# Kernel tuning notes

Hardware: AMD Instinct MI355X
Metric: run time of the kernel (lower is better)

## Reference

```python
import jax, jax.numpy as jnp
import numpy as np

N, R, H, L, E = 50000, 16, 32, 8, 1600000


def setup_inputs() -> dict:
    key = jax.random.key(0)
    ks = jax.random.split(key, 8)
    edge_index = jax.random.randint(ks[0], (2, E), 0, N, dtype=jnp.int32)
    edge_type = jax.random.randint(ks[1], (E,), 0, R, dtype=jnp.int32)
    W1 = jax.random.normal(ks[2], (R, N, H), jnp.float32) * 0.02
    root1 = jax.random.normal(ks[3], (N, H), jnp.float32) * 0.02
    b1 = jnp.zeros((H,), jnp.float32)
    W2 = jax.random.normal(ks[4], (R, H, L), jnp.float32) * 0.1
    root2 = jax.random.normal(ks[5], (H, L), jnp.float32) * 0.1
    b2 = jnp.zeros((L,), jnp.float32)
    return {"edge_index": edge_index, "edge_type": edge_type,
            "W1": W1, "root1": root1, "b1": b1,
            "W2": W2, "root2": root2, "b2": b2}


def reference(edge_index, edge_type, W1, root1, b1, W2, root2, b2):
    src, dst = edge_index[0], edge_index[1]
    # PyG RGCNConv uses mean aggregation per relation: segment = (relation, dst)
    seg = edge_type * N + dst                                   # [E]
    cnt = jax.ops.segment_sum(jnp.ones((E,), jnp.float32), seg, num_segments=R * N)
    norm_e = (1.0 / jnp.maximum(cnt, 1.0))[seg]                 # per-edge 1/deg_r(dst)

    # Layer 1: x is None -> message for edge (j->i, r) is W1[r, j]; root term is root1[i]
    msg1 = W1[edge_type, src] * norm_e[:, None]                 # [E, H]
    agg1 = jax.ops.segment_sum(msg1, dst, num_segments=N)       # [N, H]
    h1 = jax.nn.relu(agg1 + root1 + b1)

    # Layer 2: mean-aggregate h1[src] per (relation, dst), then relation-wise GEMM
    msg2 = h1[src] * norm_e[:, None]                            # [E, H]
    A = jax.ops.segment_sum(msg2, seg, num_segments=R * N).reshape(R, N, H)
    out = jnp.einsum('rnh,rhl->nl', A, W2) + h1 @ root2 + b2    # [N, L]
    return jax.nn.sigmoid(out)
```

## Files before the change

### kernel.cpp

```cpp
#include <hip/hip_runtime.h>
#include <hip/hip_bf16.h>

#define Nn 50000
#define Rr 16
#define Hh 32
#define Ll 8
#define Ee 1600000
#define NSEG 800000
#define NB 782
#define CH 4096
#define NBLK1 391
#define COLS 392
#define HT_INT4 76636
#define CAP 3072
#define W2U 20

typedef _Float16 h2 __attribute__((ext_vector_type(2)));

__device__ __forceinline__ float dot2(h2 a, unsigned b, float c) {
#ifdef __AMDGCN__
    return __builtin_amdgcn_fdot2(a, __builtin_bit_cast(h2, b), c, false);
#else
    h2 hb = __builtin_bit_cast(h2, b);
    return fmaf((float)a[0], (float)hb[0],
                fmaf((float)a[1], (float)hb[1], c));
#endif
}

__global__ __launch_bounds__(256) void p1hist_kernel(
        const int* __restrict__ dst, int* __restrict__ histT) {
    __shared__ int hist[1024];
    for (int i = threadIdx.x; i < 1024; i += 256) hist[i] = 0;
    __syncthreads();
    int base = blockIdx.x * CH;
    int n = min(CH, Ee - base);
    for (int i = threadIdx.x; i < n; i += 256)
        atomicAdd(&hist[dst[base + i] >> 6], 1);
    __syncthreads();
    for (int k = threadIdx.x; k < NB; k += 256)
        histT[k * COLS + blockIdx.x] = hist[k];
}

__global__ __launch_bounds__(256) void scan1_kernel(
        int4* data4, int* __restrict__ bsum) {
    __shared__ int sm[256];
    int i4 = blockIdx.x * 256 + threadIdx.x;
    int4 v = make_int4(0, 0, 0, 0);
    if (i4 < HT_INT4) v = data4[i4];
    int s0 = v.x, s1 = s0 + v.y, s2 = s1 + v.z, s3 = s2 + v.w;
    sm[threadIdx.x] = s3;
    __syncthreads();
    for (int off = 1; off < 256; off <<= 1) {
        int add = (threadIdx.x >= off) ? sm[threadIdx.x - off] : 0;
        __syncthreads();
        sm[threadIdx.x] += add;
        __syncthreads();
    }
    int base = sm[threadIdx.x] - s3;
    if (i4 < HT_INT4)
        data4[i4] = make_int4(base, base + s0, base + s1, base + s2);
    if (threadIdx.x == 255) bsum[blockIdx.x] = sm[255];
}

__global__ __launch_bounds__(1024) void scan2_kernel(
        const int* __restrict__ bsum, int* __restrict__ boff, int nblk) {
    __shared__ int sm[1024];
    int v = (threadIdx.x < nblk) ? bsum[threadIdx.x] : 0;
    sm[threadIdx.x] = v;
    __syncthreads();
    for (int off = 1; off < 1024; off <<= 1) {
        int add = (threadIdx.x >= off) ? sm[threadIdx.x - off] : 0;
        __syncthreads();
        sm[threadIdx.x] += add;
        __syncthreads();
    }
    if (threadIdx.x < nblk) boff[threadIdx.x] = sm[threadIdx.x] - v;
}

__global__ __launch_bounds__(256) void p1scat_kernel(
        const int* __restrict__ src, const int* __restrict__ dst,
        const int* __restrict__ etype, const int* __restrict__ offsT,
        const int* __restrict__ boff, unsigned* __restrict__ pay) {
    __shared__ int lhist[1024], lofs[1024], lcur[1024], goff[1024];
    __shared__ int partial[256];
    __shared__ unsigned stage[CH];
    __shared__ unsigned short sbkt[CH];
    int t = threadIdx.x;
    for (int i = t; i < 1024; i += 256) lhist[i] = 0;
    __syncthreads();
    int base = blockIdx.x * CH;
    int n = min(CH, Ee - base);
    for (int i = t; i < n; i += 256)
        atomicAdd(&lhist[dst[base + i] >> 6], 1);
    __syncthreads();
    int h0 = lhist[4*t], h1v = lhist[4*t+1], h2i = lhist[4*t+2], h3 = lhist[4*t+3];
    int s = h0 + h1v + h2i + h3;
    partial[t] = s;
    __syncthreads();
    for (int off = 1; off < 256; off <<= 1) {
        int add = (t >= off) ? partial[t - off] : 0;
        __syncthreads();
        partial[t] += add;
        __syncthreads();
    }
    int run = partial[t] - s;
    lofs[4*t] = run; lcur[4*t] = run; run += h0;
    lofs[4*t+1] = run; lcur[4*t+1] = run; run += h1v;
    lofs[4*t+2] = run; lcur[4*t+2] = run; run += h2i;
    lofs[4*t+3] = run; lcur[4*t+3] = run;
    for (int k = t; k < NB; k += 256) {
        int idx = k * COLS + blockIdx.x;
        goff[k] = offsT[idx] + boff[idx >> 10];
    }
    __syncthreads();
    for (int i = t; i < n; i += 256) {
        int e = base + i;
        int dv = dst[e];
        int b = dv >> 6;
        int pos = atomicAdd(&lcur[b], 1);
        stage[pos] = ((unsigned)(dv & 63) << 20) | ((unsigned)etype[e] << 16)
                   | (unsigned)src[e];
        sbkt[pos] = (unsigned short)b;
    }
    __syncthreads();
    for (int j = t; j < n; j += 256) {
        int b = sbkt[j];
        pay[goff[b] + (j - lofs[b])] = stage[j];
    }
}

__global__ __launch_bounds__(256) void p2sort_kernel(
        const int* __restrict__ offsT, const int* __restrict__ boff,
        unsigned* pay, unsigned* __restrict__ combo) {
    __shared__ unsigned buf[CAP], outb[CAP];
    __shared__ int hist[1024], lofs[1024], lcur[1024], partial[256];
    int k = blockIdx.x, t = threadIdx.x;
    int idx0 = k * COLS;
    int base = offsT[idx0] + boff[idx0 >> 10];
    int next;
    if (k == NB - 1) {
        next = Ee;
    } else {
        int idx1 = (k + 1) * COLS;
        next = offsT[idx1] + boff[idx1 >> 10];
    }
    int n = next - base;
    for (int i = t; i < 1024; i += 256) hist[i] = 0;
    __syncthreads();
    for (int j = t; j < n; j += 256) {
        unsigned p = pay[base + j];
        buf[j] = p;
        atomicAdd(&hist[(p >> 16) & 0x3FFu], 1);
    }
    __syncthreads();
    int h0 = hist[4*t], h1v = hist[4*t+1], h2i = hist[4*t+2], h3 = hist[4*t+3];
    int s = h0 + h1v + h2i + h3;
    partial[t] = s;
    __syncthreads();
    for (int off = 1; off < 256; off <<= 1) {
        int add = (t >= off) ? partial[t - off] : 0;
        __syncthreads();
        partial[t] += add;
        __syncthreads();
    }
    int run = partial[t] - s;
    lofs[4*t] = run; lcur[4*t] = run; run += h0;
    lofs[4*t+1] = run; lcur[4*t+1] = run; run += h1v;
    lofs[4*t+2] = run; lcur[4*t+2] = run; run += h2i;
    lofs[4*t+3] = run; lcur[4*t+3] = run;
    __syncthreads();
    for (int bin = t; bin < 1024; bin += 256) {
        int dglob = (k << 6) | (bin >> 4);
        if (dglob < Nn)
            combo[(k << 10) | bin] =
                ((unsigned)(base + lofs[bin]) << 8) | (unsigned)hist[bin];
    }
    if (k == NB - 1 && t == 0) combo[NSEG] = ((unsigned)Ee) << 8;
    for (int j = t; j < n; j += 256) {
        unsigned p = buf[j];
        int bin = (int)((p >> 16) & 0x3FFu);
        int pos = atomicAdd(&lcur[bin], 1);
        outb[pos] = (((p >> 16) & 15u) << 24) | ((unsigned)hist[bin] << 16)
                  | (p & 0xFFFFu);
    }
    __syncthreads();
    for (int j = t; j < n; j += 256) pay[base + j] = outb[j];
}

__global__ __launch_bounds__(256) void layer1_kernel(
        const unsigned* __restrict__ csr32, const unsigned* __restrict__ combo,
        const float* __restrict__ W1, const float* __restrict__ root1,
        const float* __restrict__ b1, unsigned short* __restrict__ h1h) {
    int d = (blockIdx.x * 256 + threadIdx.x) >> 6;
    int lane = threadIdx.x & 63;
    int slot = lane >> 3, chunk = lane & 7;
    if (d >= Nn) return;
    int beg = (int)(combo[d << 4] >> 8);
    int end = (int)(combo[(d + 1) << 4] >> 8);
    int deg = end - beg;
    float4 acc = make_float4(0.f, 0.f, 0.f, 0.f);
    const float* Wc = W1 + (chunk << 2);
#pragma unroll 1
    for (int i = 0; i < deg; i += 32) {
        int p0 = i + slot, p1 = p0 + 8, p2 = p0 + 16, p3 = p0 + 24;
        bool r0 = p0 < deg, r1 = p1 < deg, r2 = p2 < deg, r3 = p3 < deg;
        unsigned v0 = csr32[beg + (r0 ? p0 : 0)];
        unsigned v1 = csr32[beg + (r1 ? p1 : 0)];
        unsigned v2 = csr32[beg + (r2 ? p2 : 0)];
        unsigned v3 = csr32[beg + (r3 ? p3 : 0)];
        float n0 = r0 ? __builtin_amdgcn_rcpf((float)((v0 >> 16) & 255u)) : 0.f;
        float n1 = r1 ? __builtin_amdgcn_rcpf((float)((v1 >> 16) & 255u)) : 0.f;
        float n2 = r2 ? __builtin_amdgcn_rcpf((float)((v2 >> 16) & 255u)) : 0.f;
        float n3 = r3 ? __builtin_amdgcn_rcpf((float)((v3 >> 16) & 255u)) : 0.f;
        float4 w0 = *(const float4*)(Wc +
            ((size_t)((int)(v0 >> 24) * Nn + (int)(v0 & 0xffffu)) << 5));
        float4 w1 = *(const float4*)(Wc +
            ((size_t)((int)(v1 >> 24) * Nn + (int)(v1 & 0xffffu)) << 5));
        float4 w2 = *(const float4*)(Wc +
            ((size_t)((int)(v2 >> 24) * Nn + (int)(v2 & 0xffffu)) << 5));
        float4 w3 = *(const float4*)(Wc +
            ((size_t)((int)(v3 >> 24) * Nn + (int)(v3 & 0xffffu)) << 5));
        acc.x = fmaf(n0, w0.x, acc.x); acc.y = fmaf(n0, w0.y, acc.y);
        acc.z = fmaf(n0, w0.z, acc.z); acc.w = fmaf(n0, w0.w, acc.w);
        acc.x = fmaf(n1, w1.x, acc.x); acc.y = fmaf(n1, w1.y, acc.y);
        acc.z = fmaf(n1, w1.z, acc.z); acc.w = fmaf(n1, w1.w, acc.w);
        acc.x = fmaf(n2, w2.x, acc.x); acc.y = fmaf(n2, w2.y, acc.y);
        acc.z = fmaf(n2, w2.z, acc.z); acc.w = fmaf(n2, w2.w, acc.w);
        acc.x = fmaf(n3, w3.x, acc.x); acc.y = fmaf(n3, w3.y, acc.y);
        acc.z = fmaf(n3, w3.z, acc.z); acc.w = fmaf(n3, w3.w, acc.w);
    }
#pragma unroll
    for (int m = 8; m <= 32; m <<= 1) {
        acc.x += __shfl_xor(acc.x, m, 64);
        acc.y += __shfl_xor(acc.y, m, 64);
        acc.z += __shfl_xor(acc.z, m, 64);
        acc.w += __shfl_xor(acc.w, m, 64);
    }
    if (slot == 0) {
        int hb = chunk << 2;
        float4 rt = *(const float4*)(root1 + (d << 5) + hb);
        float4 bb = *(const float4*)(b1 + hb);
        _Float16 q0 = (_Float16)fmaxf(acc.x + rt.x + bb.x, 0.f);
        _Float16 q1 = (_Float16)fmaxf(acc.y + rt.y + bb.y, 0.f);
        _Float16 q2 = (_Float16)fmaxf(acc.z + rt.z + bb.z, 0.f);
        _Float16 q3 = (_Float16)fmaxf(acc.w + rt.w + bb.w, 0.f);
        ushort4 ov;
        ov.x = __builtin_bit_cast(unsigned short, q0);
        ov.y = __builtin_bit_cast(unsigned short, q1);
        ov.z = __builtin_bit_cast(unsigned short, q2);
        ov.w = __builtin_bit_cast(unsigned short, q3);
        *(ushort4*)(h1h + (d << 5) + hb) = ov;
    }
}

__global__ __launch_bounds__(256) void layer2_kernel(
        const unsigned* __restrict__ csr32, const unsigned* __restrict__ combo,
        const unsigned short* __restrict__ h1h, const float* __restrict__ W2,
        const float* __restrict__ root2, const float* __restrict__ b2,
        float* __restrict__ out) {
    __shared__ unsigned W2s[17 * 8 * W2U];
    for (int idx = threadIdx.x; idx < 17 * 8 * 16; idx += 256) {
        int r = idx >> 7;
        int c = (idx >> 4) & 7;
        int u = idx & 15;
        int hp = u >> 3, l = u & 7;
        int hh = (c << 2) | (hp << 1);
        float w0, w1;
        if (r < 16) {
            w0 = W2[(r << 8) + (hh << 3) + l];
            w1 = W2[(r << 8) + ((hh + 1) << 3) + l];
        } else {
            w0 = root2[(hh << 3) + l];
            w1 = root2[((hh + 1) << 3) + l];
        }
        h2 p = { (_Float16)w0, (_Float16)w1 };
        W2s[((r << 3) | c) * W2U + u] = __builtin_bit_cast(unsigned, p);
    }
    __syncthreads();

    int d = (blockIdx.x * 256 + threadIdx.x) >> 6;
    int lane = threadIdx.x & 63;
    int slot = lane >> 3, chunk = lane & 7;
    if (d >= Nn) return;
    int beg = (int)(combo[d << 4] >> 8);
    int end = (int)(combo[(d + 1) << 4] >> 8);
    int deg = end - beg;
    int degv = deg + 1;
    float acc[8] = {0.f, 0.f, 0.f, 0.f, 0.f, 0.f, 0.f, 0.f};
    const int hb = chunk << 2;
#pragma unroll 1
    for (int i = 0; i < degv; i += 32) {
        int p0 = i + slot, p1 = p0 + 8, p2 = p0 + 16, p3 = p0 + 24;
        bool re0 = p0 < deg, re1 = p1 < deg, re2 = p2 < deg, re3 = p3 < deg;
        bool vi0 = p0 == deg, vi1 = p1 == deg, vi2 = p2 == deg, vi3 = p3 == deg;
        unsigned v0 = csr32[beg + (re0 ? p0 : 0)];
        unsigned v1 = csr32[beg + (re1 ? p1 : 0)];
        unsigned v2 = csr32[beg + (re2 ? p2 : 0)];
        unsigned v3 = csr32[beg + (re3 ? p3 : 0)];
        int s0 = vi0 ? d : (re0 ? (int)(v0 & 0xffffu) : 0);
        int s1 = vi1 ? d : (re1 ? (int)(v1 & 0xffffu) : 0);
        int s2 = vi2 ? d : (re2 ? (int)(v2 & 0xffffu) : 0);
        int s3 = vi3 ? d : (re3 ? (int)(v3 & 0xffffu) : 0);
        int r0 = vi0 ? 16 : (re0 ? (int)(v0 >> 24) : 0);
        int r1 = vi1 ? 16 : (re1 ? (int)(v1 >> 24) : 0);
        int r2 = vi2 ? 16 : (re2 ? (int)(v2 >> 24) : 0);
        int r3 = vi3 ? 16 : (re3 ? (int)(v3 >> 24) : 0);
        float n0 = vi0 ? 1.0f
                 : (re0 ? __builtin_amdgcn_rcpf((float)((v0 >> 16) & 255u)) : 0.f);
        float n1 = vi1 ? 1.0f
                 : (re1 ? __builtin_amdgcn_rcpf((float)((v1 >> 16) & 255u)) : 0.f);
        float n2 = vi2 ? 1.0f
                 : (re2 ? __builtin_amdgcn_rcpf((float)((v2 >> 16) & 255u)) : 0.f);
        float n3 = vi3 ? 1.0f
                 : (re3 ? __builtin_amdgcn_rcpf((float)((v3 >> 16) & 255u)) : 0.f);
        uint2 hw0 = *(const uint2*)(h1h + (s0 << 5) + hb);
        uint2 hw1 = *(const uint2*)(h1h + (s1 << 5) + hb);
        uint2 hw2 = *(const uint2*)(h1h + (s2 << 5) + hb);
        uint2 hw3 = *(const uint2*)(h1h + (s3 << 5) + hb);
        const unsigned* w0p = &W2s[((r0 << 3) | chunk) * W2U];
        const unsigned* w1p = &W2s[((r1 << 3) | chunk) * W2U];
        const unsigned* w2p = &W2s[((r2 << 3) | chunk) * W2U];
        const unsigned* w3p = &W2s[((r3 << 3) | chunk) * W2U];

        h2 n0h = { (_Float16)n0, (_Float16)n0 };
        h2 a00 = __builtin_bit_cast(h2, hw0.x) * n0h;
        h2 a01 = __builtin_bit_cast(h2, hw0.y) * n0h;
        uint4 b00 = *(const uint4*)(w0p);
        uint4 b01 = *(const uint4*)(w0p + 4);
        uint4 b02 = *(const uint4*)(w0p + 8);
        uint4 b03 = *(const uint4*)(w0p + 12);
        acc[0] = dot2(a00, b00.x, acc[0]); acc[1] = dot2(a00, b00.y, acc[1]);
        acc[2] = dot2(a00, b00.z, acc[2]); acc[3] = dot2(a00, b00.w, acc[3]);
        acc[4] = dot2(a00, b01.x, acc[4]); acc[5] = dot2(a00, b01.y, acc[5]);
        acc[6] = dot2(a00, b01.z, acc[6]); acc[7] = dot2(a00, b01.w, acc[7]);
        acc[0] = dot2(a01, b02.x, acc[0]); acc[1] = dot2(a01, b02.y, acc[1]);
        acc[2] = dot2(a01, b02.z, acc[2]); acc[3] = dot2(a01, b02.w, acc[3]);
        acc[4] = dot2(a01, b03.x, acc[4]); acc[5] = dot2(a01, b03.y, acc[5]);
        acc[6] = dot2(a01, b03.z, acc[6]); acc[7] = dot2(a01, b03.w, acc[7]);

        h2 n1h = { (_Float16)n1, (_Float16)n1 };
        h2 a10 = __builtin_bit_cast(h2, hw1.x) * n1h;
        h2 a11 = __builtin_bit_cast(h2, hw1.y) * n1h;
        uint4 b10 = *(const uint4*)(w1p);
        uint4 b11 = *(const uint4*)(w1p + 4);
        uint4 b12 = *(const uint4*)(w1p + 8);
        uint4 b13 = *(const uint4*)(w1p + 12);
        acc[0] = dot2(a10, b10.x, acc[0]); acc[1] = dot2(a10, b10.y, acc[1]);
        acc[2] = dot2(a10, b10.z, acc[2]); acc[3] = dot2(a10, b10.w, acc[3]);
        acc[4] = dot2(a10, b11.x, acc[4]); acc[5] = dot2(a10, b11.y, acc[5]);
        acc[6] = dot2(a10, b11.z, acc[6]); acc[7] = dot2(a10, b11.w, acc[7]);
        acc[0] = dot2(a11, b12.x, acc[0]); acc[1] = dot2(a11, b12.y, acc[1]);
        acc[2] = dot2(a11, b12.z, acc[2]); acc[3] = dot2(a11, b12.w, acc[3]);
        acc[4] = dot2(a11, b13.x, acc[4]); acc[5] = dot2(a11, b13.y, acc[5]);
        acc[6] = dot2(a11, b13.z, acc[6]); acc[7] = dot2(a11, b13.w, acc[7]);

        h2 n2h = { (_Float16)n2, (_Float16)n2 };
        h2 a20 = __builtin_bit_cast(h2, hw2.x) * n2h;
        h2 a21 = __builtin_bit_cast(h2, hw2.y) * n2h;
        uint4 b20 = *(const uint4*)(w2p);
        uint4 b21 = *(const uint4*)(w2p + 4);
        uint4 b22 = *(const uint4*)(w2p + 8);
        uint4 b23 = *(const uint4*)(w2p + 12);
        acc[0] = dot2(a20, b20.x, acc[0]); acc[1] = dot2(a20, b20.y, acc[1]);
        acc[2] = dot2(a20, b20.z, acc[2]); acc[3] = dot2(a20, b20.w, acc[3]);
        acc[4] = dot2(a20, b21.x, acc[4]); acc[5] = dot2(a20, b21.y, acc[5]);
        acc[6] = dot2(a20, b21.z, acc[6]); acc[7] = dot2(a20, b21.w, acc[7]);
        acc[0] = dot2(a21, b22.x, acc[0]); acc[1] = dot2(a21, b22.y, acc[1]);
        acc[2] = dot2(a21, b22.z, acc[2]); acc[3] = dot2(a21, b22.w, acc[3]);
        acc[4] = dot2(a21, b23.x, acc[4]); acc[5] = dot2(a21, b23.y, acc[5]);
        acc[6] = dot2(a21, b23.z, acc[6]); acc[7] = dot2(a21, b23.w, acc[7]);

        h2 n3h = { (_Float16)n3, (_Float16)n3 };
        h2 a30 = __builtin_bit_cast(h2, hw3.x) * n3h;
        h2 a31 = __builtin_bit_cast(h2, hw3.y) * n3h;
        uint4 b30 = *(const uint4*)(w3p);
        uint4 b31 = *(const uint4*)(w3p + 4);
        uint4 b32 = *(const uint4*)(w3p + 8);
        uint4 b33 = *(const uint4*)(w3p + 12);
        acc[0] = dot2(a30, b30.x, acc[0]); acc[1] = dot2(a30, b30.y, acc[1]);
        acc[2] = dot2(a30, b30.z, acc[2]); acc[3] = dot2(a30, b30.w, acc[3]);
        acc[4] = dot2(a30, b31.x, acc[4]); acc[5] = dot2(a30, b31.y, acc[5]);
        acc[6] = dot2(a30, b31.z, acc[6]); acc[7] = dot2(a30, b31.w, acc[7]);
        acc[0] = dot2(a31, b32.x, acc[0]); acc[1] = dot2(a31, b32.y, acc[1]);
        acc[2] = dot2(a31, b32.z, acc[2]); acc[3] = dot2(a31, b32.w, acc[3]);
        acc[4] = dot2(a31, b33.x, acc[4]); acc[5] = dot2(a31, b33.y, acc[5]);
        acc[6] = dot2(a31, b33.z, acc[6]); acc[7] = dot2(a31, b33.w, acc[7]);
    }
#pragma unroll
    for (int m = 1; m <= 32; m <<= 1) {
#pragma unroll
        for (int l = 0; l < 8; ++l)
            acc[l] += __shfl_xor(acc[l], m, 64);
    }
    if (lane < 8) {
        float myv = acc[0];
#pragma unroll
        for (int l = 1; l < 8; ++l) myv = (lane == l) ? acc[l] : myv;
        float o = myv + b2[lane];
        out[(d << 3) | lane] = 1.0f / (1.0f + __expf(-o));
    }
}

extern "C" void kernel_launch(void* const* d_in, const int* in_sizes, int n_in,
                              void* d_out, int out_size, void* d_ws, size_t ws_size,
                              hipStream_t stream) {
    const int* edge_index = (const int*)d_in[0];
    const int* etype      = (const int*)d_in[1];
    const float* W1    = (const float*)d_in[2];
    const float* root1 = (const float*)d_in[3];
    const float* b1    = (const float*)d_in[4];
    const float* W2    = (const float*)d_in[5];
    const float* root2 = (const float*)d_in[6];
    const float* b2    = (const float*)d_in[7];
    float* out = (float*)d_out;

    const int* src = edge_index;
    const int* dst = edge_index + Ee;

    int* ws = (int*)d_ws;
    unsigned* combo        = (unsigned*)ws;
    unsigned* pay          = (unsigned*)(ws + 800016);
    unsigned short* h1h    = (unsigned short*)(ws + 2400016);
    int* histT             = ws + 3200016;
    int* bsum              = ws + 3506560;
    int* boff              = ws + 3506872;

    if (ws_size < (size_t)3507184 * sizeof(int)) return;

    hipMemsetAsync(histT, 0, (size_t)(NB * COLS) * sizeof(int), stream);

    const int nblkSc = (HT_INT4 + 255) / 256;
    const int nblkL  = (Nn * 64 + 255) / 256;

    p1hist_kernel<<<NBLK1, 256, 0, stream>>>(dst, histT);
    scan1_kernel<<<nblkSc, 256, 0, stream>>>((int4*)histT, bsum);
    scan2_kernel<<<1, 1024, 0, stream>>>(bsum, boff, nblkSc);
    p1scat_kernel<<<NBLK1, 256, 0, stream>>>(src, dst, etype, histT, boff, pay);
    p2sort_kernel<<<NB, 256, 0, stream>>>(histT, boff, pay, combo);
    layer1_kernel<<<nblkL, 256, 0, stream>>>(pay, combo, W1, root1, b1, h1h);
    layer2_kernel<<<nblkL, 256, 0, stream>>>(pay, combo, h1h, W2, root2, b2, out);
}
```

Before: 298.6 us.

## Replace two-pass bucketed LDS sort with global-atomic counting sort by segment

```diff
diff --git a/kernel.cpp b/kernel.cpp
--- a/kernel.cpp
+++ b/kernel.cpp
@@ -7,12 +7,8 @@
 #define Ll 8
 #define Ee 1600000
 #define NSEG 800000
-#define NB 782
-#define CH 4096
-#define NBLK1 391
-#define COLS 392
-#define HT_INT4 76636
-#define CAP 3072
+#define NI4 200000
+#define NBLK_SC 782
 #define W2U 20
 
 typedef _Float16 h2 __attribute__((ext_vector_type(2)));
@@ -27,26 +23,25 @@
 #endif
 }
 
-__global__ __launch_bounds__(256) void p1hist_kernel(
-        const int* __restrict__ dst, int* __restrict__ histT) {
-    __shared__ int hist[1024];
-    for (int i = threadIdx.x; i < 1024; i += 256) hist[i] = 0;
-    __syncthreads();
-    int base = blockIdx.x * CH;
-    int n = min(CH, Ee - base);
-    for (int i = threadIdx.x; i < n; i += 256)
-        atomicAdd(&hist[dst[base + i] >> 6], 1);
-    __syncthreads();
-    for (int k = threadIdx.x; k < NB; k += 256)
-        histT[k * COLS + blockIdx.x] = hist[k];
-}
-
-__global__ __launch_bounds__(256) void scan1_kernel(
+__global__ __launch_bounds__(256) void count_kernel(
+        const int* __restrict__ dst, const int* __restrict__ etype,
+        int* __restrict__ counts) {
+    int i = blockIdx.x * 256 + threadIdx.x;
+    if (i >= Ee / 4) return;
+    int4 d4 = ((const int4*)dst)[i];
+    int4 e4 = ((const int4*)etype)[i];
+    atomicAdd(&counts[(d4.x << 4) | e4.x], 1);
+    atomicAdd(&counts[(d4.y << 4) | e4.y], 1);
+    atomicAdd(&counts[(d4.z << 4) | e4.z], 1);
+    atomicAdd(&counts[(d4.w << 4) | e4.w], 1);
+}
+
+__global__ __launch_bounds__(256) void scanA_kernel(
         int4* data4, int* __restrict__ bsum) {
     __shared__ int sm[256];
     int i4 = blockIdx.x * 256 + threadIdx.x;
     int4 v = make_int4(0, 0, 0, 0);
-    if (i4 < HT_INT4) v = data4[i4];
+    if (i4 < NI4) v = data4[i4];
     int s0 = v.x, s1 = s0 + v.y, s2 = s1 + v.z, s3 = s2 + v.w;
     sm[threadIdx.x] = s3;
     __syncthreads();
@@ -57,12 +52,12 @@
         __syncthreads();
     }
     int base = sm[threadIdx.x] - s3;
-    if (i4 < HT_INT4)
+    if (i4 < NI4)
         data4[i4] = make_int4(base, base + s0, base + s1, base + s2);
     if (threadIdx.x == 255) bsum[blockIdx.x] = sm[255];
 }
 
-__global__ __launch_bounds__(1024) void scan2_kernel(
+__global__ __launch_bounds__(1024) void scanB_kernel(
         const int* __restrict__ bsum, int* __restrict__ boff, int nblk) {
     __shared__ int sm[1024];
     int v = (threadIdx.x < nblk) ? bsum[threadIdx.x] : 0;
@@ -77,114 +72,63 @@
     if (threadIdx.x < nblk) boff[threadIdx.x] = sm[threadIdx.x] - v;
 }
 
-__global__ __launch_bounds__(256) void p1scat_kernel(
+__global__ __launch_bounds__(256) void fixup_kernel(
+        const int4* __restrict__ data4, const int* __restrict__ boff,
+        unsigned* __restrict__ combo, int* __restrict__ cur) {
+    int i4 = blockIdx.x * 256 + threadIdx.x;
+    if (i4 >= NI4) return;
+    int b = boff[i4 >> 8];
+    int4 v = data4[i4];
+    int o0 = v.x + b, o1 = v.y + b, o2 = v.z + b, o3 = v.w + b;
+    int o4;
+    if (i4 == NI4 - 1) {
+        o4 = Ee;
+    } else {
+        int nb = boff[(i4 + 1) >> 8];
+        o4 = data4[i4 + 1].x + nb;
+    }
+    int s = i4 << 2;
+    combo[s]     = ((unsigned)o0 << 8) | (unsigned)(o1 - o0);
+    combo[s + 1] = ((unsigned)o1 << 8) | (unsigned)(o2 - o1);
+    combo[s + 2] = ((unsigned)o2 << 8) | (unsigned)(o3 - o2);
+    combo[s + 3] = ((unsigned)o3 << 8) | (unsigned)(o4 - o3);
+    ((int4*)cur)[i4] = make_int4(o0, o1, o2, o3);
+    if (i4 == 0) combo[NSEG] = ((unsigned)Ee) << 8;
+}
+
+__global__ __launch_bounds__(256) void scatter_kernel(
         const int* __restrict__ src, const int* __restrict__ dst,
-        const int* __restrict__ etype, const int* __restrict__ offsT,
-        const int* __restrict__ boff, unsigned* __restrict__ pay) {
-    __shared__ int lhist[1024], lofs[1024], lcur[1024], goff[1024];
-    __shared__ int partial[256];
-    __shared__ unsigned stage[CH];
-    __shared__ unsigned short sbkt[CH];
-    int t = threadIdx.x;
-    for (int i = t; i < 1024; i += 256) lhist[i] = 0;
-    __syncthreads();
-    int base = blockIdx.x * CH;
-    int n = min(CH, Ee - base);
-    for (int i = t; i < n; i += 256)
-        atomicAdd(&lhist[dst[base + i] >> 6], 1);
-    __syncthreads();
-    int h0 = lhist[4*t], h1v = lhist[4*t+1], h2i = lhist[4*t+2], h3 = lhist[4*t+3];
-    int s = h0 + h1v + h2i + h3;
-    partial[t] = s;
-    __syncthreads();
-    for (int off = 1; off < 256; off <<= 1) {
-        int add = (t >= off) ? partial[t - off] : 0;
-        __syncthreads();
-        partial[t] += add;
-        __syncthreads();
-    }
-    int run = partial[t] - s;
-    lofs[4*t] = run; lcur[4*t] = run; run += h0;
-    lofs[4*t+1] = run; lcur[4*t+1] = run; run += h1v;
-    lofs[4*t+2] = run; lcur[4*t+2] = run; run += h2i;
-    lofs[4*t+3] = run; lcur[4*t+3] = run;
-    for (int k = t; k < NB; k += 256) {
-        int idx = k * COLS + blockIdx.x;
-        goff[k] = offsT[idx] + boff[idx >> 10];
-    }
-    __syncthreads();
-    for (int i = t; i < n; i += 256) {
-        int e = base + i;
-        int dv = dst[e];
-        int b = dv >> 6;
-        int pos = atomicAdd(&lcur[b], 1);
-        stage[pos] = ((unsigned)(dv & 63) << 20) | ((unsigned)etype[e] << 16)
-                   | (unsigned)src[e];
-        sbkt[pos] = (unsigned short)b;
-    }
-    __syncthreads();
-    for (int j = t; j < n; j += 256) {
-        int b = sbkt[j];
-        pay[goff[b] + (j - lofs[b])] = stage[j];
-    }
-}
-
-__global__ __launch_bounds__(256) void p2sort_kernel(
-        const int* __restrict__ offsT, const int* __restrict__ boff,
-        unsigned* pay, unsigned* __restrict__ combo) {
-    __shared__ unsigned buf[CAP], outb[CAP];
-    __shared__ int hist[1024], lofs[1024], lcur[1024], partial[256];
-    int k = blockIdx.x, t = threadIdx.x;
-    int idx0 = k * COLS;
-    int base = offsT[idx0] + boff[idx0 >> 10];
-    int next;
-    if (k == NB - 1) {
-        next = Ee;
-    } else {
-        int idx1 = (k + 1) * COLS;
-        next = offsT[idx1] + boff[idx1 >> 10];
-    }
-    int n = next - base;
-    for (int i = t; i < 1024; i += 256) hist[i] = 0;
-    __syncthreads();
-    for (int j = t; j < n; j += 256) {
-        unsigned p = pay[base + j];
-        buf[j] = p;
-        atomicAdd(&hist[(p >> 16) & 0x3FFu], 1);
-    }
-    __syncthreads();
-    int h0 = hist[4*t], h1v = hist[4*t+1], h2i = hist[4*t+2], h3 = hist[4*t+3];
-    int s = h0 + h1v + h2i + h3;
-    partial[t] = s;
-    __syncthreads();
-    for (int off = 1; off < 256; off <<= 1) {
-        int add = (t >= off) ? partial[t - off] : 0;
-        __syncthreads();
-        partial[t] += add;
-        __syncthreads();
-    }
-    int run = partial[t] - s;
-    lofs[4*t] = run; lcur[4*t] = run; run += h0;
-    lofs[4*t+1] = run; lcur[4*t+1] = run; run += h1v;
-    lofs[4*t+2] = run; lcur[4*t+2] = run; run += h2i;
-    lofs[4*t+3] = run; lcur[4*t+3] = run;
-    __syncthreads();
-    for (int bin = t; bin < 1024; bin += 256) {
-        int dglob = (k << 6) | (bin >> 4);
-        if (dglob < Nn)
-            combo[(k << 10) | bin] =
-                ((unsigned)(base + lofs[bin]) << 8) | (unsigned)hist[bin];
-    }
-    if (k == NB - 1 && t == 0) combo[NSEG] = ((unsigned)Ee) << 8;
-    for (int j = t; j < n; j += 256) {
-        unsigned p = buf[j];
-        int bin = (int)((p >> 16) & 0x3FFu);
-        int pos = atomicAdd(&lcur[bin], 1);
-        outb[pos] = (((p >> 16) & 15u) << 24) | ((unsigned)hist[bin] << 16)
-                  | (p & 0xFFFFu);
-    }
-    __syncthreads();
-    for (int j = t; j < n; j += 256) pay[base + j] = outb[j];
+        const int* __restrict__ etype, const unsigned* __restrict__ combo,
+        int* __restrict__ cur, unsigned* __restrict__ csr32) {
+    int i = blockIdx.x * 256 + threadIdx.x;
+    if (i >= Ee / 4) return;
+    int4 s4 = ((const int4*)src)[i];
+    int4 d4 = ((const int4*)dst)[i];
+    int4 e4 = ((const int4*)etype)[i];
+    {
+        int seg = (d4.x << 4) | e4.x;
+        int pos = atomicAdd(&cur[seg], 1);
+        unsigned cnt = combo[seg] & 255u;
+        csr32[pos] = ((unsigned)e4.x << 24) | (cnt << 16) | (unsigned)s4.x;
+    }
+    {
+        int seg = (d4.y << 4) | e4.y;
+        int pos = atomicAdd(&cur[seg], 1);
+        unsigned cnt = combo[seg] & 255u;
+        csr32[pos] = ((unsigned)e4.y << 24) | (cnt << 16) | (unsigned)s4.y;
+    }
+    {
+        int seg = (d4.z << 4) | e4.z;
+        int pos = atomicAdd(&cur[seg], 1);
+        unsigned cnt = combo[seg] & 255u;
+        csr32[pos] = ((unsigned)e4.z << 24) | (cnt << 16) | (unsigned)s4.z;
+    }
+    {
+        int seg = (d4.w << 4) | e4.w;
+        int pos = atomicAdd(&cur[seg], 1);
+        unsigned cnt = combo[seg] & 255u;
+        csr32[pos] = ((unsigned)e4.w << 24) | (cnt << 16) | (unsigned)s4.w;
+    }
 }
 
 __global__ __launch_bounds__(256) void layer1_kernel(
@@ -419,24 +363,28 @@
 
     int* ws = (int*)d_ws;
     unsigned* combo        = (unsigned*)ws;
-    unsigned* pay          = (unsigned*)(ws + 800016);
+    unsigned* csr32        = (unsigned*)(ws + 800016);
     unsigned short* h1h    = (unsigned short*)(ws + 2400016);
-    int* histT             = ws + 3200016;
-    int* bsum              = ws + 3506560;
-    int* boff              = ws + 3506872;
-
-    if (ws_size < (size_t)3507184 * sizeof(int)) return;
-
-    hipMemsetAsync(histT, 0, (size_t)(NB * COLS) * sizeof(int), stream);
-
-    const int nblkSc = (HT_INT4 + 255) / 256;
+    int* counts            = ws + 3200016;
+    int* cur               = ws + 4000016;
+    int* bsum              = ws + 4800016;
+    int* boff              = ws + 4801040;
+
+    if (ws_size < (size_t)4802064 * sizeof(int)) return;
+
+    hipMemsetAsync(counts, 0, (size_t)NSEG * sizeof(int), stream);
+
+    const int nblkE  = (Ee / 4 + 255) / 256;
     const int nblkL  = (Nn * 64 + 255) / 256;
 
-    p1hist_kernel<<<NBLK1, 256, 0, stream>>>(dst, histT);
-    scan1_kernel<<<nblkSc, 256, 0, stream>>>((int4*)histT, bsum);
-    scan2_kernel<<<1, 1024, 0, stream>>>(bsum, boff, nblkSc);
-    p1scat_kernel<<<NBLK1, 256, 0, stream>>>(src, dst, etype, histT, boff, pay);
-    p2sort_kernel<<<NB, 256, 0, stream>>>(histT, boff, pay, combo);
-    layer1_kernel<<<nblkL, 256, 0, stream>>>(pay, combo, W1, root1, b1, h1h);
-    layer2_kernel<<<nblkL, 256, 0, stream>>>(pay, combo, h1h, W2, root2, b2, out);
-}
+    count_kernel<<<nblkE, 256, 0, stream>>>(dst, etype, counts);
+    scanA_kernel<<<NBLK_SC, 256, 0, stream>>>((int4*)counts, bsum);
+    scanB_kernel<<<1, 1024, 0, stream>>>(bsum, boff, NBLK_SC);
+    fixup_kernel<<<NBLK_SC, 256, 0, stream>>>((const int4*)counts, boff,
+                                              combo, cur);
+    scatter_kernel<<<nblkE, 256, 0, stream>>>(src, dst, etype, combo, cur,
+                                              csr32);
+    layer1_kernel<<<nblkL, 256, 0, stream>>>(csr32, combo, W1, root1, b1, h1h);
+    layer2_kernel<<<nblkL, 256, 0, stream>>>(csr32, combo, h1h, W2, root2, b2,
+                                             out);
+}
```

Result: slower. 395.1 us (+32.3%).
